# Performance work log

Hardware: AMD Instinct MI355X
Metric: run time of the kernel (lower is better)

The kernel has to match this reference:

```python
import jax, jax.numpy as jnp
import numpy as np

# Dimensions
B, N_PER_MOL = 256, 64            # molecules, atoms per molecule (equal-split case of tf.split)
N = B * N_PER_MOL                 # total atoms
P = 131072                        # total pairs (edges)
D_ATOM, D_PAIR = 256, 64
C = 128                           # num_clusters
H = 50                            # WeaveLayer default hidden sizes (AA=PA=AP=PP=50)
H_A = 2 * H                       # n_hidden_A = n_hidden_AA + n_hidden_PA


def _glorot(key, shape):
    fan_in, fan_out = shape
    lim = jnp.sqrt(6.0 / (fan_in + fan_out)).astype(jnp.float32)
    return jax.random.uniform(key, shape, jnp.float32, -lim, lim)


def setup_inputs() -> dict:
    key = jax.random.key(0)
    ks = jax.random.split(key, 12)
    atom_features = jax.random.normal(ks[0], (N, D_ATOM), jnp.float32)
    pair_features = jax.random.normal(ks[1], (P, D_PAIR), jnp.float32)
    pair_split = jax.random.randint(ks[2], (P,), 0, N, jnp.int32)
    atom_to_pair = jax.random.randint(ks[3], (P, 2), 0, N, jnp.int32)
    num_atoms = jnp.full((B,), N_PER_MOL, dtype=jnp.int32)  # equal-sized molecules
    params = {
        "W_aa": _glorot(ks[4], (D_ATOM, H_A)), "b_aa": jnp.zeros((H_A,), jnp.float32),
        "W_pa": _glorot(ks[5], (D_PAIR, H)),   "b_pa": jnp.zeros((H,), jnp.float32),
        "W_ao": _glorot(ks[6], (H_A + H, C)),  "b_ao": jnp.zeros((C,), jnp.float32),
        "W_ap": _glorot(ks[7], (2 * D_ATOM, H)), "b_ap": jnp.zeros((H,), jnp.float32),
        "W_pp": _glorot(ks[8], (D_PAIR, H)),   "b_pp": jnp.zeros((H,), jnp.float32),
        "W_po": _glorot(ks[9], (2 * H, D_PAIR)), "b_po": jnp.zeros((D_PAIR,), jnp.float32),
    }
    return dict(atom_features=atom_features, pair_features=pair_features,
                pair_split=pair_split, atom_to_pair=atom_to_pair,
                num_atoms=num_atoms, **params)


def reference(atom_features, pair_features, pair_split, atom_to_pair, num_atoms,
              W_aa, b_aa, W_pa, b_pa, W_ao, b_ao, W_ap, b_ap, W_pp, b_pp, W_po, b_po):
    relu = jax.nn.relu
    n_atoms, d_atom = atom_features.shape
    n_mols = num_atoms.shape[0]
    n_per = n_atoms // n_mols  # equal-sized molecules (static)

    # --- WeaveLayer atom path ---
    AA = relu(atom_features @ W_aa + b_aa)                              # [N, 100]
    PA = relu(pair_features @ W_pa + b_pa)                              # [P, 50]
    PA = jax.ops.segment_sum(PA, pair_split, num_segments=n_atoms)     # [N, 50]
    A = relu(jnp.concatenate([AA, PA], axis=-1) @ W_ao + b_ao)          # [N, C] assign logits

    # --- WeaveLayer pair path (computed by the original layer) ---
    ap_ij = atom_features[atom_to_pair].reshape(-1, 2 * d_atom)         # [P, 2D]
    ap_ji = atom_features[atom_to_pair[:, ::-1]].reshape(-1, 2 * d_atom)
    AP = relu(ap_ij @ W_ap + b_ap) + relu(ap_ji @ W_ap + b_ap)          # [P, 50]
    PP = relu(pair_features @ W_pp + b_pp)                              # [P, 50]
    P_out = relu(jnp.concatenate([AP, PP], axis=-1) @ W_po + b_po)      # [P, pair_dim]

    # --- DiffPool: softmax assignment + per-molecule S^T X pooling ---
    assign = jax.nn.softmax(A, axis=-1)                                 # [N, C]
    S = assign.reshape(n_mols, n_per, -1)                               # [B, n, C]
    X = atom_features.reshape(n_mols, n_per, d_atom)                    # [B, n, D]
    pooled = jnp.einsum('bnc,bnd->bcd', S, X)                           # [B, C, D]
    return pooled, P_out
```

## Files before the change

### kernel.cpp

```cpp
#include <hip/hip_runtime.h>
#include <hip/hip_bf16.h>

#define N_ATOMS 16384
#define N_PAIRS 131072

#define OFF_PA    0
#define OFF_PASEG 6815744
#define OFF_AA    7634944
#define OFF_U     9273344
#define OFF_V     10125312
#define OFF_S     10977280
#define OFF_IDX   13074432
#define OFF_OFS   13205504
#define OFF_CNT   13221890

__global__ __launch_bounds__(256) void k0_count(const int* __restrict__ split,
                                                int* __restrict__ cnt)
{
    int p = blockIdx.x * 256 + threadIdx.x;
    atomicAdd(&cnt[split[p]], 1);
}

__global__ __launch_bounds__(1024) void k_scan(int* __restrict__ cnt,
                                               int* __restrict__ ofs)
{
    __shared__ int part[1024];
    const int t = threadIdx.x;
    const int base = t * 16;
    int v[16];
    int s = 0;
    #pragma unroll
    for (int i = 0; i < 16; ++i) { v[i] = cnt[base + i]; s += v[i]; }
    part[t] = s;
    __syncthreads();
    for (int off = 1; off < 1024; off <<= 1) {
        int x = (t >= off) ? part[t - off] : 0;
        __syncthreads();
        part[t] += x;
        __syncthreads();
    }
    int excl = part[t] - s;
    #pragma unroll
    for (int i = 0; i < 16; ++i) {
        int c = v[i];
        ofs[base + i] = excl;
        cnt[base + i] = excl;
        excl += c;
    }
    if (t == 1023) ofs[16384] = excl;
}

__global__ __launch_bounds__(256) void k0_fill(const int* __restrict__ split,
                                               int* __restrict__ cur,
                                               int* __restrict__ idx)
{
    int p = blockIdx.x * 256 + threadIdx.x;
    int pos = atomicAdd(&cur[split[p]], 1);
    idx[pos] = p;
}

__global__ __launch_bounds__(256, 2) void k1_atom(
    const float* __restrict__ X,
    const float* __restrict__ Waa, const float* __restrict__ baa,
    const float* __restrict__ Wap,
    float* __restrict__ AA, float* __restrict__ U, float* __restrict__ V)
{
    __shared__ __align__(16) float xt[256][20];
    const int t = threadIdx.x;
    const int a0 = blockIdx.x * 16;
    #pragma unroll
    for (int r = 0; r < 16; ++r) {
        xt[t][r] = X[(size_t)(a0 + r) * 256 + t];
    }
    __syncthreads();
    const int c = t;
    if (c < 200) {
        const float* wp; int stride; float bias = 0.f;
        if (c < 100)      { wp = Waa + c;                  stride = 100; bias = baa[c]; }
        else if (c < 150) { wp = Wap + (c - 100);          stride = 50; }
        else              { wp = Wap + 256*50 + (c - 150); stride = 50; }
        float acc[16];
        #pragma unroll
        for (int a = 0; a < 16; ++a) acc[a] = bias;
        #pragma unroll 4
        for (int k = 0; k < 256; ++k) {
            float w = wp[(size_t)k * stride];
            const float4* xr = (const float4*)&xt[k][0];
            #pragma unroll
            for (int a4 = 0; a4 < 4; ++a4) {
                float4 x = xr[a4];
                acc[a4*4+0] = fmaf(x.x, w, acc[a4*4+0]);
                acc[a4*4+1] = fmaf(x.y, w, acc[a4*4+1]);
                acc[a4*4+2] = fmaf(x.z, w, acc[a4*4+2]);
                acc[a4*4+3] = fmaf(x.w, w, acc[a4*4+3]);
            }
        }
        if (c < 100) {
            #pragma unroll
            for (int a = 0; a < 16; ++a)
                AA[(size_t)(a0 + a) * 100 + c] = fmaxf(acc[a], 0.f);
        } else if (c < 150) {
            #pragma unroll
            for (int a = 0; a < 16; ++a)
                U[(size_t)(a0 + a) * 52 + (c - 100)] = acc[a];
        } else {
            #pragma unroll
            for (int a = 0; a < 16; ++a)
                V[(size_t)(a0 + a) * 52 + (c - 150)] = acc[a];
        }
    } else if (c == 200) {
        #pragma unroll
        for (int a = 0; a < 16; ++a) {
            U[(size_t)(a0 + a) * 52 + 50] = 0.f;
            U[(size_t)(a0 + a) * 52 + 51] = 0.f;
        }
    } else if (c == 201) {
        #pragma unroll
        for (int a = 0; a < 16; ++a) {
            V[(size_t)(a0 + a) * 52 + 50] = 0.f;
            V[(size_t)(a0 + a) * 52 + 51] = 0.f;
        }
    }
}

__global__ __launch_bounds__(256, 2) void k2a_pa(
    const float* __restrict__ PF,
    const float* __restrict__ Wpa, const float* __restrict__ bpa,
    float* __restrict__ PAo)
{
    __shared__ __align__(16) float Wc[64][52];
    __shared__ __align__(16) float bc[52];
    const int t = threadIdx.x;
    for (int i = t; i < 64 * 52; i += 256) {
        int k = i / 52, c = i % 52;
        Wc[k][c] = (c < 50) ? Wpa[k * 50 + c] : 0.f;
    }
    if (t < 52) bc[t] = (t < 50) ? bpa[t] : 0.f;
    __syncthreads();
    const int p = blockIdx.x * 256 + t;
    float acc[52];
    #pragma unroll
    for (int c = 0; c < 52; ++c) acc[c] = bc[c];
    const float4* pf4 = (const float4*)(PF + (size_t)p * 64);
    #pragma unroll 2
    for (int k4 = 0; k4 < 16; ++k4) {
        float4 xv = pf4[k4];
        float xs[4] = {xv.x, xv.y, xv.z, xv.w};
        #pragma unroll
        for (int kk = 0; kk < 4; ++kk) {
            const float4* wr = (const float4*)&Wc[k4*4 + kk][0];
            float x = xs[kk];
            #pragma unroll
            for (int c4 = 0; c4 < 13; ++c4) {
                float4 w = wr[c4];
                acc[c4*4+0] = fmaf(x, w.x, acc[c4*4+0]);
                acc[c4*4+1] = fmaf(x, w.y, acc[c4*4+1]);
                acc[c4*4+2] = fmaf(x, w.z, acc[c4*4+2]);
                acc[c4*4+3] = fmaf(x, w.w, acc[c4*4+3]);
            }
        }
    }
    float4* op = (float4*)(PAo + (size_t)p * 52);
    #pragma unroll
    for (int q = 0; q < 13; ++q) {
        op[q] = make_float4(fmaxf(acc[4*q+0], 0.f), fmaxf(acc[4*q+1], 0.f),
                            fmaxf(acc[4*q+2], 0.f), fmaxf(acc[4*q+3], 0.f));
    }
}

__global__ __launch_bounds__(256) void k_seg(
    const float* __restrict__ PAo, const int* __restrict__ idx,
    const int* __restrict__ ofs, float* __restrict__ PAseg)
{
    const int t = threadIdx.x;
    const int a = blockIdx.x * 4 + (t >> 6);
    const int lane = t & 63;
    const int beg = ofs[a], end = ofs[a + 1];
    const int cn = end - beg;
    int pre = (lane < cn) ? idx[beg + lane] : 0;
    float s = 0.f;
    for (int j = 0; j < cn; ++j) {
        int p = (j < 64) ? __shfl(pre, j, 64) : idx[beg + j];
        if (lane < 50) s += PAo[(size_t)p * 52 + lane];
    }
    if (lane < 50) PAseg[(size_t)a * 50 + lane] = s;
}

__global__ __launch_bounds__(256, 2) void k2b_pair_out(
    const int* __restrict__ a2p,
    const float* __restrict__ U, const float* __restrict__ V,
    const float* __restrict__ bap_g,
    const float* __restrict__ PF,
    const float* __restrict__ Wpp, const float* __restrict__ bpp_g,
    const float* __restrict__ Wpo, const float* __restrict__ bpo,
    float* __restrict__ Pout)
{
    __shared__ __align__(16) float Wo[100][32];
    __shared__ __align__(16) float Wp[64][52];
    __shared__ __align__(16) float bap[52];
    __shared__ __align__(16) float bpp[52];
    __shared__ float bo[32];
    const int t = threadIdx.x;
    const int h = blockIdx.x & 1;
    const int pb = blockIdx.x >> 1;
    for (int i = t; i < 3200; i += 256)
        Wo[i >> 5][i & 31] = Wpo[(size_t)(i >> 5) * 64 + h * 32 + (i & 31)];
    for (int i = t; i < 64 * 52; i += 256) {
        int k = i / 52, c = i % 52;
        Wp[k][c] = (c < 50) ? Wpp[k * 50 + c] : 0.f;
    }
    if (t < 52) bap[t] = (t < 50) ? bap_g[t] : 0.f;
    if (t < 52) bpp[t] = (t < 50) ? bpp_g[t] : 0.f;
    if (t < 32) bo[t] = bpo[h * 32 + t];
    __syncthreads();
    const int p = pb * 256 + t;

    float pp[52];
    #pragma unroll
    for (int c = 0; c < 52; ++c) pp[c] = bpp[c];
    {
        const float4* pf4 = (const float4*)(PF + (size_t)p * 64);
        #pragma unroll 2
        for (int k4 = 0; k4 < 16; ++k4) {
            float4 xv = pf4[k4];
            float xs[4] = {xv.x, xv.y, xv.z, xv.w};
            #pragma unroll
            for (int kk = 0; kk < 4; ++kk) {
                const float4* wr = (const float4*)&Wp[k4*4 + kk][0];
                float x = xs[kk];
                #pragma unroll
                for (int c4 = 0; c4 < 13; ++c4) {
                    float4 w = wr[c4];
                    pp[c4*4+0] = fmaf(x, w.x, pp[c4*4+0]);
                    pp[c4*4+1] = fmaf(x, w.y, pp[c4*4+1]);
                    pp[c4*4+2] = fmaf(x, w.z, pp[c4*4+2]);
                    pp[c4*4+3] = fmaf(x, w.w, pp[c4*4+3]);
                }
            }
        }
        #pragma unroll
        for (int c = 0; c < 52; ++c) pp[c] = fmaxf(pp[c], 0.f);
    }

    float ap[52];
    {
        const int2 ij = ((const int2*)a2p)[p];
        const float4* Ui = (const float4*)(U + (size_t)ij.x * 52);
        const float4* Vi = (const float4*)(V + (size_t)ij.x * 52);
        const float4* Uj = (const float4*)(U + (size_t)ij.y * 52);
        const float4* Vj = (const float4*)(V + (size_t)ij.y * 52);
        #pragma unroll
        for (int c4 = 0; c4 < 13; ++c4) {
            float4 ui = Ui[c4], vj = Vj[c4], uj = Uj[c4], vi = Vi[c4];
            const float4 bb = *(const float4*)&bap[c4*4];
            ap[c4*4+0] = fmaxf(ui.x + vj.x + bb.x, 0.f) + fmaxf(uj.x + vi.x + bb.x, 0.f);
            ap[c4*4+1] = fmaxf(ui.y + vj.y + bb.y, 0.f) + fmaxf(uj.y + vi.y + bb.y, 0.f);
            ap[c4*4+2] = fmaxf(ui.z + vj.z + bb.z, 0.f) + fmaxf(uj.z + vi.z + bb.z, 0.f);
            ap[c4*4+3] = fmaxf(ui.w + vj.w + bb.w, 0.f) + fmaxf(uj.w + vi.w + bb.w, 0.f);
        }
    }

    float o[32];
    #pragma unroll
    for (int c = 0; c < 32; ++c) o[c] = bo[c];
    #pragma unroll
    for (int k = 0; k < 50; ++k) {
        float a = ap[k];
        const float4* wr = (const float4*)&Wo[k][0];
        #pragma unroll
        for (int c4 = 0; c4 < 8; ++c4) {
            float4 w = wr[c4];
            o[c4*4+0] = fmaf(a, w.x, o[c4*4+0]);
            o[c4*4+1] = fmaf(a, w.y, o[c4*4+1]);
            o[c4*4+2] = fmaf(a, w.z, o[c4*4+2]);
            o[c4*4+3] = fmaf(a, w.w, o[c4*4+3]);
        }
    }
    #pragma unroll
    for (int k = 0; k < 50; ++k) {
        float a = pp[k];
        const float4* wr = (const float4*)&Wo[50 + k][0];
        #pragma unroll
        for (int c4 = 0; c4 < 8; ++c4) {
            float4 w = wr[c4];
            o[c4*4+0] = fmaf(a, w.x, o[c4*4+0]);
            o[c4*4+1] = fmaf(a, w.y, o[c4*4+1]);
            o[c4*4+2] = fmaf(a, w.z, o[c4*4+2]);
            o[c4*4+3] = fmaf(a, w.w, o[c4*4+3]);
        }
    }
    float4* outp = (float4*)(Pout + (size_t)p * 64 + h * 32);
    #pragma unroll
    for (int q = 0; q < 8; ++q) {
        outp[q] = make_float4(fmaxf(o[4*q+0], 0.f), fmaxf(o[4*q+1], 0.f),
                              fmaxf(o[4*q+2], 0.f), fmaxf(o[4*q+3], 0.f));
    }
}

__global__ __launch_bounds__(256, 2) void k3_assign(
    const float* __restrict__ AA, const float* __restrict__ PAseg,
    const float* __restrict__ Wao, const float* __restrict__ bao,
    float* __restrict__ S)
{
    __shared__ __align__(16) float featT[150][16];
    __shared__ __align__(16) float L[16][128];
    const int t = threadIdx.x;
    const int a0 = blockIdx.x * 16;
    for (int idx = t; idx < 2400; idx += 256) {
        int a = idx / 150, k = idx % 150;
        featT[k][a] = (k < 100) ? AA[(size_t)(a0 + a) * 100 + k]
                                : PAseg[(size_t)(a0 + a) * 50 + (k - 100)];
    }
    __syncthreads();
    const int c = t & 127, g = t >> 7;
    float acc[8];
    float b = bao[c];
    #pragma unroll
    for (int a = 0; a < 8; ++a) acc[a] = b;
    #pragma unroll 2
    for (int k = 0; k < 150; ++k) {
        float w = Wao[(size_t)k * 128 + c];
        const float4* fr = (const float4*)&featT[k][g * 8];
        float4 f0 = fr[0], f1 = fr[1];
        acc[0] = fmaf(f0.x, w, acc[0]); acc[1] = fmaf(f0.y, w, acc[1]);
        acc[2] = fmaf(f0.z, w, acc[2]); acc[3] = fmaf(f0.w, w, acc[3]);
        acc[4] = fmaf(f1.x, w, acc[4]); acc[5] = fmaf(f1.y, w, acc[5]);
        acc[6] = fmaf(f1.z, w, acc[6]); acc[7] = fmaf(f1.w, w, acc[7]);
    }
    #pragma unroll
    for (int a = 0; a < 8; ++a) L[g*8 + a][c] = fmaxf(acc[a], 0.f);
    __syncthreads();
    const int r = t & 15, a = t >> 4;
    float v[8];
    #pragma unroll
    for (int q = 0; q < 8; ++q) v[q] = L[a][r + 16*q];
    float m = v[0];
    #pragma unroll
    for (int q = 1; q < 8; ++q) m = fmaxf(m, v[q]);
    #pragma unroll
    for (int w = 1; w < 16; w <<= 1) m = fmaxf(m, __shfl_xor(m, w, 64));
    float e[8];
    float s = 0.f;
    #pragma unroll
    for (int q = 0; q < 8; ++q) { e[q] = __expf(v[q] - m); s += e[q]; }
    #pragma unroll
    for (int w = 1; w < 16; w <<= 1) s += __shfl_xor(s, w, 64);
    float inv = 1.f / s;
    #pragma unroll
    for (int q = 0; q < 8; ++q)
        S[(size_t)(a0 + a) * 128 + r + 16*q] = e[q] * inv;
}

__global__ __launch_bounds__(256, 2) void k4_pool(
    const float* __restrict__ X, const float* __restrict__ S,
    float* __restrict__ pooled)
{
    __shared__ __align__(16) float Sl[64][128];
    __shared__ __align__(16) float Xl[64][64];
    const int t = threadIdx.x;
    const int b = blockIdx.x >> 2;
    const int doff = (blockIdx.x & 3) * 64;
    for (int i = t; i < 8192; i += 256) {
        int n = i >> 7, cd = i & 127;
        Sl[n][cd] = S[(size_t)(b*64 + n) * 128 + cd];
    }
    for (int i = t; i < 4096; i += 256) {
        int n = i >> 6, cd = i & 63;
        Xl[n][cd] = X[(size_t)(b*64 + n) * 256 + doff + cd];
    }
    __syncthreads();
    const int c = t & 127, dq = t >> 7;
    float4 f[8];
    #pragma unroll
    for (int q = 0; q < 8; ++q) f[q] = make_float4(0.f, 0.f, 0.f, 0.f);
    #pragma unroll 2
    for (int n = 0; n < 64; ++n) {
        float s = Sl[n][c];
        const float4* xr = (const float4*)&Xl[n][dq * 32];
        #pragma unroll
        for (int q = 0; q < 8; ++q) {
            float4 x = xr[q];
            f[q].x = fmaf(s, x.x, f[q].x);
            f[q].y = fmaf(s, x.y, f[q].y);
            f[q].z = fmaf(s, x.z, f[q].z);
            f[q].w = fmaf(s, x.w, f[q].w);
        }
    }
    size_t base = (size_t)b * 32768 + (size_t)c * 256 + doff + dq * 32;
    float4* op = (float4*)(pooled + base);
    #pragma unroll
    for (int q = 0; q < 8; ++q) op[q] = f[q];
}

extern "C" void kernel_launch(void* const* d_in, const int* in_sizes, int n_in,
                              void* d_out, int out_size, void* d_ws, size_t ws_size,
                              hipStream_t stream)
{
    const float* atom = (const float*)d_in[0];
    const float* pair = (const float*)d_in[1];
    const int*   split = (const int*)d_in[2];
    const int*   a2p  = (const int*)d_in[3];
    const float* Waa = (const float*)d_in[5];
    const float* baa = (const float*)d_in[6];
    const float* Wpa = (const float*)d_in[7];
    const float* bpa = (const float*)d_in[8];
    const float* Wao = (const float*)d_in[9];
    const float* bao = (const float*)d_in[10];
    const float* Wap = (const float*)d_in[11];
    const float* bap = (const float*)d_in[12];
    const float* Wpp = (const float*)d_in[13];
    const float* bpp = (const float*)d_in[14];
    const float* Wpo = (const float*)d_in[15];
    const float* bpo = (const float*)d_in[16];

    float* ws = (float*)d_ws;
    float* PAo   = ws + OFF_PA;
    float* PAseg = ws + OFF_PASEG;
    float* AA = ws + OFF_AA;
    float* U  = ws + OFF_U;
    float* V  = ws + OFF_V;
    float* Sm = ws + OFF_S;
    int* idx = (int*)(ws + OFF_IDX);
    int* ofs = (int*)(ws + OFF_OFS);
    int* cnt = (int*)(ws + OFF_CNT);

    float* pooled = (float*)d_out;
    float* Pout = pooled + (size_t)256 * 128 * 256;

    hipMemsetAsync(cnt, 0, N_ATOMS * sizeof(int), stream);
    k0_count<<<512, 256, 0, stream>>>(split, cnt);
    k_scan<<<1, 1024, 0, stream>>>(cnt, ofs);
    k0_fill<<<512, 256, 0, stream>>>(split, cnt, idx);
    k1_atom<<<1024, 256, 0, stream>>>(atom, Waa, baa, Wap, AA, U, V);
    k2a_pa<<<512, 256, 0, stream>>>(pair, Wpa, bpa, PAo);
    k_seg<<<4096, 256, 0, stream>>>(PAo, idx, ofs, PAseg);
    k2b_pair_out<<<1024, 256, 0, stream>>>(a2p, U, V, bap, pair, Wpp, bpp, Wpo, bpo, Pout);
    k3_assign<<<1024, 256, 0, stream>>>(AA, PAseg, Wao, bao, Sm);
    k4_pool<<<1024, 256, 0, stream>>>(atom, Sm, pooled);
}
```

Baseline: 427.4 us.

## Drop LDS staging, read weights and activations from global/cache, pre-pad weights once

Removes shared-memory staging from several kernels (atom matmul, pair projections, assign, pool) and reads weights and inputs straight from global memory, relying on cache and uniform loads. Padded copies of the pair weights and biases are built once in the scan kernel instead of in every block. The pair-output kernel now computes both output halves per thread, which halves the grid and avoids recomputing the PP and AP terms twice. The risk is that uncoalesced or strided global reads (e.g. AA and PAseg row reads in assign, per-thread X rows in k1) replace cheap LDS reads, and register pressure rises.

```diff
diff --git a/kernel.cpp b/kernel.cpp
--- a/kernel.cpp
+++ b/kernel.cpp
@@ -13,6 +13,11 @@
 #define OFF_IDX   13074432
 #define OFF_OFS   13205504
 #define OFF_CNT   13221890
+#define OFF_WPAP  13238288
+#define OFF_WPPP  13241616
+#define OFF_BPAP  13244944
+#define OFF_BAPP  13245008
+#define OFF_BPPP  13245072
 
 __global__ __launch_bounds__(256) void k0_count(const int* __restrict__ split,
                                                 int* __restrict__ cnt)
@@ -21,8 +26,13 @@
     atomicAdd(&cnt[split[p]], 1);
 }
 
-__global__ __launch_bounds__(1024) void k_scan(int* __restrict__ cnt,
-                                               int* __restrict__ ofs)
+__global__ __launch_bounds__(1024) void k_scan(
+    int* __restrict__ cnt, int* __restrict__ ofs,
+    const float* __restrict__ Wpa, const float* __restrict__ bpa,
+    const float* __restrict__ Wpp, const float* __restrict__ bpp,
+    const float* __restrict__ bap,
+    float* __restrict__ WpaP, float* __restrict__ WppP,
+    float* __restrict__ BpaP, float* __restrict__ BppP, float* __restrict__ BapP)
 {
     __shared__ int part[1024];
     const int t = threadIdx.x;
@@ -48,6 +58,16 @@
         excl += c;
     }
     if (t == 1023) ofs[16384] = excl;
+    for (int i = t; i < 64 * 52; i += 1024) {
+        int k = i / 52, c = i % 52;
+        WpaP[i] = (c < 50) ? Wpa[k * 50 + c] : 0.f;
+        WppP[i] = (c < 50) ? Wpp[k * 50 + c] : 0.f;
+    }
+    if (t < 52) {
+        BpaP[t] = (t < 50) ? bpa[t] : 0.f;
+        BppP[t] = (t < 50) ? bpp[t] : 0.f;
+        BapP[t] = (t < 50) ? bap[t] : 0.f;
+    }
 }
 
 __global__ __launch_bounds__(256) void k0_fill(const int* __restrict__ split,
@@ -59,100 +79,93 @@
     idx[pos] = p;
 }
 
-__global__ __launch_bounds__(256, 2) void k1_atom(
+__global__ __launch_bounds__(256) void k1_atom(
     const float* __restrict__ X,
     const float* __restrict__ Waa, const float* __restrict__ baa,
     const float* __restrict__ Wap,
     float* __restrict__ AA, float* __restrict__ U, float* __restrict__ V)
 {
-    __shared__ __align__(16) float xt[256][20];
     const int t = threadIdx.x;
     const int a0 = blockIdx.x * 16;
-    #pragma unroll
-    for (int r = 0; r < 16; ++r) {
-        xt[t][r] = X[(size_t)(a0 + r) * 256 + t];
-    }
-    __syncthreads();
     const int c = t;
-    if (c < 200) {
-        const float* wp; int stride; float bias = 0.f;
-        if (c < 100)      { wp = Waa + c;                  stride = 100; bias = baa[c]; }
-        else if (c < 150) { wp = Wap + (c - 100);          stride = 50; }
-        else              { wp = Wap + 256*50 + (c - 150); stride = 50; }
-        float acc[16];
-        #pragma unroll
-        for (int a = 0; a < 16; ++a) acc[a] = bias;
-        #pragma unroll 4
-        for (int k = 0; k < 256; ++k) {
-            float w = wp[(size_t)k * stride];
-            const float4* xr = (const float4*)&xt[k][0];
-            #pragma unroll
-            for (int a4 = 0; a4 < 4; ++a4) {
-                float4 x = xr[a4];
-                acc[a4*4+0] = fmaf(x.x, w, acc[a4*4+0]);
-                acc[a4*4+1] = fmaf(x.y, w, acc[a4*4+1]);
-                acc[a4*4+2] = fmaf(x.z, w, acc[a4*4+2]);
-                acc[a4*4+3] = fmaf(x.w, w, acc[a4*4+3]);
-            }
-        }
-        if (c < 100) {
-            #pragma unroll
-            for (int a = 0; a < 16; ++a)
-                AA[(size_t)(a0 + a) * 100 + c] = fmaxf(acc[a], 0.f);
-        } else if (c < 150) {
-            #pragma unroll
-            for (int a = 0; a < 16; ++a)
-                U[(size_t)(a0 + a) * 52 + (c - 100)] = acc[a];
-        } else {
-            #pragma unroll
-            for (int a = 0; a < 16; ++a)
-                V[(size_t)(a0 + a) * 52 + (c - 150)] = acc[a];
-        }
-    } else if (c == 200) {
+    if (c >= 202) return;
+    if (c == 200) {
         #pragma unroll
         for (int a = 0; a < 16; ++a) {
             U[(size_t)(a0 + a) * 52 + 50] = 0.f;
             U[(size_t)(a0 + a) * 52 + 51] = 0.f;
         }
-    } else if (c == 201) {
+        return;
+    }
+    if (c == 201) {
         #pragma unroll
         for (int a = 0; a < 16; ++a) {
             V[(size_t)(a0 + a) * 52 + 50] = 0.f;
             V[(size_t)(a0 + a) * 52 + 51] = 0.f;
         }
-    }
-}
-
-__global__ __launch_bounds__(256, 2) void k2a_pa(
+        return;
+    }
+    const float* wp; int stride; float bias = 0.f;
+    if (c < 100)      { wp = Waa + c;                  stride = 100; bias = baa[c]; }
+    else if (c < 150) { wp = Wap + (c - 100);          stride = 50; }
+    else              { wp = Wap + 256*50 + (c - 150); stride = 50; }
+    float acc[16];
+    #pragma unroll
+    for (int a = 0; a < 16; ++a) acc[a] = bias;
+    for (int k4 = 0; k4 < 64; ++k4) {
+        float4 xq[16];
+        #pragma unroll
+        for (int r = 0; r < 16; ++r)
+            xq[r] = *(const float4*)(X + (size_t)(a0 + r) * 256 + k4 * 4);
+        #pragma unroll
+        for (int kk = 0; kk < 4; ++kk) {
+            float w = wp[(size_t)(k4 * 4 + kk) * stride];
+            #pragma unroll
+            for (int r = 0; r < 16; ++r) {
+                float xv = (kk == 0) ? xq[r].x : (kk == 1) ? xq[r].y
+                         : (kk == 2) ? xq[r].z : xq[r].w;
+                acc[r] = fmaf(xv, w, acc[r]);
+            }
+        }
+    }
+    if (c < 100) {
+        #pragma unroll
+        for (int a = 0; a < 16; ++a)
+            AA[(size_t)(a0 + a) * 100 + c] = fmaxf(acc[a], 0.f);
+    } else if (c < 150) {
+        #pragma unroll
+        for (int a = 0; a < 16; ++a)
+            U[(size_t)(a0 + a) * 52 + (c - 100)] = acc[a];
+    } else {
+        #pragma unroll
+        for (int a = 0; a < 16; ++a)
+            V[(size_t)(a0 + a) * 52 + (c - 150)] = acc[a];
+    }
+}
+
+__global__ __launch_bounds__(256) void k2a_pa(
     const float* __restrict__ PF,
-    const float* __restrict__ Wpa, const float* __restrict__ bpa,
+    const float* __restrict__ WpaP, const float* __restrict__ BpaP,
     float* __restrict__ PAo)
 {
-    __shared__ __align__(16) float Wc[64][52];
-    __shared__ __align__(16) float bc[52];
-    const int t = threadIdx.x;
-    for (int i = t; i < 64 * 52; i += 256) {
-        int k = i / 52, c = i % 52;
-        Wc[k][c] = (c < 50) ? Wpa[k * 50 + c] : 0.f;
-    }
-    if (t < 52) bc[t] = (t < 50) ? bpa[t] : 0.f;
-    __syncthreads();
+    const int t = threadIdx.x;
     const int p = blockIdx.x * 256 + t;
     float acc[52];
     #pragma unroll
-    for (int c = 0; c < 52; ++c) acc[c] = bc[c];
+    for (int c4 = 0; c4 < 13; ++c4) {
+        float4 b = *(const float4*)(BpaP + c4 * 4);
+        acc[c4*4+0] = b.x; acc[c4*4+1] = b.y; acc[c4*4+2] = b.z; acc[c4*4+3] = b.w;
+    }
     const float4* pf4 = (const float4*)(PF + (size_t)p * 64);
-    #pragma unroll 2
     for (int k4 = 0; k4 < 16; ++k4) {
         float4 xv = pf4[k4];
-        float xs[4] = {xv.x, xv.y, xv.z, xv.w};
         #pragma unroll
         for (int kk = 0; kk < 4; ++kk) {
-            const float4* wr = (const float4*)&Wc[k4*4 + kk][0];
-            float x = xs[kk];
+            float x = (kk == 0) ? xv.x : (kk == 1) ? xv.y : (kk == 2) ? xv.z : xv.w;
+            const float* wr = WpaP + (k4 * 4 + kk) * 52;
             #pragma unroll
             for (int c4 = 0; c4 < 13; ++c4) {
-                float4 w = wr[c4];
+                float4 w = *(const float4*)(wr + c4 * 4);
                 acc[c4*4+0] = fmaf(x, w.x, acc[c4*4+0]);
                 acc[c4*4+1] = fmaf(x, w.y, acc[c4*4+1]);
                 acc[c4*4+2] = fmaf(x, w.z, acc[c4*4+2]);
@@ -189,48 +202,32 @@
 __global__ __launch_bounds__(256, 2) void k2b_pair_out(
     const int* __restrict__ a2p,
     const float* __restrict__ U, const float* __restrict__ V,
-    const float* __restrict__ bap_g,
+    const float* __restrict__ BapP,
     const float* __restrict__ PF,
-    const float* __restrict__ Wpp, const float* __restrict__ bpp_g,
+    const float* __restrict__ WppP, const float* __restrict__ BppP,
     const float* __restrict__ Wpo, const float* __restrict__ bpo,
     float* __restrict__ Pout)
 {
-    __shared__ __align__(16) float Wo[100][32];
-    __shared__ __align__(16) float Wp[64][52];
-    __shared__ __align__(16) float bap[52];
-    __shared__ __align__(16) float bpp[52];
-    __shared__ float bo[32];
-    const int t = threadIdx.x;
-    const int h = blockIdx.x & 1;
-    const int pb = blockIdx.x >> 1;
-    for (int i = t; i < 3200; i += 256)
-        Wo[i >> 5][i & 31] = Wpo[(size_t)(i >> 5) * 64 + h * 32 + (i & 31)];
-    for (int i = t; i < 64 * 52; i += 256) {
-        int k = i / 52, c = i % 52;
-        Wp[k][c] = (c < 50) ? Wpp[k * 50 + c] : 0.f;
-    }
-    if (t < 52) bap[t] = (t < 50) ? bap_g[t] : 0.f;
-    if (t < 52) bpp[t] = (t < 50) ? bpp_g[t] : 0.f;
-    if (t < 32) bo[t] = bpo[h * 32 + t];
-    __syncthreads();
-    const int p = pb * 256 + t;
+    const int t = threadIdx.x;
+    const int p = blockIdx.x * 256 + t;
 
     float pp[52];
     #pragma unroll
-    for (int c = 0; c < 52; ++c) pp[c] = bpp[c];
+    for (int c4 = 0; c4 < 13; ++c4) {
+        float4 b = *(const float4*)(BppP + c4 * 4);
+        pp[c4*4+0] = b.x; pp[c4*4+1] = b.y; pp[c4*4+2] = b.z; pp[c4*4+3] = b.w;
+    }
     {
         const float4* pf4 = (const float4*)(PF + (size_t)p * 64);
-        #pragma unroll 2
         for (int k4 = 0; k4 < 16; ++k4) {
             float4 xv = pf4[k4];
-            float xs[4] = {xv.x, xv.y, xv.z, xv.w};
             #pragma unroll
             for (int kk = 0; kk < 4; ++kk) {
-                const float4* wr = (const float4*)&Wp[k4*4 + kk][0];
-                float x = xs[kk];
+                float x = (kk == 0) ? xv.x : (kk == 1) ? xv.y : (kk == 2) ? xv.z : xv.w;
+                const float* wr = WppP + (k4 * 4 + kk) * 52;
                 #pragma unroll
                 for (int c4 = 0; c4 < 13; ++c4) {
-                    float4 w = wr[c4];
+                    float4 w = *(const float4*)(wr + c4 * 4);
                     pp[c4*4+0] = fmaf(x, w.x, pp[c4*4+0]);
                     pp[c4*4+1] = fmaf(x, w.y, pp[c4*4+1]);
                     pp[c4*4+2] = fmaf(x, w.z, pp[c4*4+2]);
@@ -252,7 +249,7 @@
         #pragma unroll
         for (int c4 = 0; c4 < 13; ++c4) {
             float4 ui = Ui[c4], vj = Vj[c4], uj = Uj[c4], vi = Vi[c4];
-            const float4 bb = *(const float4*)&bap[c4*4];
+            const float4 bb = *(const float4*)(BapP + c4 * 4);
             ap[c4*4+0] = fmaxf(ui.x + vj.x + bb.x, 0.f) + fmaxf(uj.x + vi.x + bb.x, 0.f);
             ap[c4*4+1] = fmaxf(ui.y + vj.y + bb.y, 0.f) + fmaxf(uj.y + vi.y + bb.y, 0.f);
             ap[c4*4+2] = fmaxf(ui.z + vj.z + bb.z, 0.f) + fmaxf(uj.z + vi.z + bb.z, 0.f);
@@ -260,40 +257,46 @@
         }
     }
 
-    float o[32];
-    #pragma unroll
-    for (int c = 0; c < 32; ++c) o[c] = bo[c];
-    #pragma unroll
-    for (int k = 0; k < 50; ++k) {
-        float a = ap[k];
-        const float4* wr = (const float4*)&Wo[k][0];
-        #pragma unroll
-        for (int c4 = 0; c4 < 8; ++c4) {
-            float4 w = wr[c4];
-            o[c4*4+0] = fmaf(a, w.x, o[c4*4+0]);
-            o[c4*4+1] = fmaf(a, w.y, o[c4*4+1]);
-            o[c4*4+2] = fmaf(a, w.z, o[c4*4+2]);
-            o[c4*4+3] = fmaf(a, w.w, o[c4*4+3]);
-        }
-    }
-    #pragma unroll
-    for (int k = 0; k < 50; ++k) {
-        float a = pp[k];
-        const float4* wr = (const float4*)&Wo[50 + k][0];
-        #pragma unroll
-        for (int c4 = 0; c4 < 8; ++c4) {
-            float4 w = wr[c4];
-            o[c4*4+0] = fmaf(a, w.x, o[c4*4+0]);
-            o[c4*4+1] = fmaf(a, w.y, o[c4*4+1]);
-            o[c4*4+2] = fmaf(a, w.z, o[c4*4+2]);
-            o[c4*4+3] = fmaf(a, w.w, o[c4*4+3]);
-        }
-    }
-    float4* outp = (float4*)(Pout + (size_t)p * 64 + h * 32);
-    #pragma unroll
-    for (int q = 0; q < 8; ++q) {
-        outp[q] = make_float4(fmaxf(o[4*q+0], 0.f), fmaxf(o[4*q+1], 0.f),
-                              fmaxf(o[4*q+2], 0.f), fmaxf(o[4*q+3], 0.f));
+    float4* outp = (float4*)(Pout + (size_t)p * 64);
+    #pragma unroll 1
+    for (int h = 0; h < 2; ++h) {
+        float o[32];
+        #pragma unroll
+        for (int q = 0; q < 8; ++q) {
+            float4 b = *(const float4*)(bpo + h * 32 + q * 4);
+            o[q*4+0] = b.x; o[q*4+1] = b.y; o[q*4+2] = b.z; o[q*4+3] = b.w;
+        }
+        #pragma unroll
+        for (int k = 0; k < 50; ++k) {
+            float a = ap[k];
+            const float* wr = Wpo + k * 64 + h * 32;
+            #pragma unroll
+            for (int c4 = 0; c4 < 8; ++c4) {
+                float4 w = *(const float4*)(wr + c4 * 4);
+                o[c4*4+0] = fmaf(a, w.x, o[c4*4+0]);
+                o[c4*4+1] = fmaf(a, w.y, o[c4*4+1]);
+                o[c4*4+2] = fmaf(a, w.z, o[c4*4+2]);
+                o[c4*4+3] = fmaf(a, w.w, o[c4*4+3]);
+            }
+        }
+        #pragma unroll
+        for (int k = 0; k < 50; ++k) {
+            float a = pp[k];
+            const float* wr = Wpo + (50 + k) * 64 + h * 32;
+            #pragma unroll
+            for (int c4 = 0; c4 < 8; ++c4) {
+                float4 w = *(const float4*)(wr + c4 * 4);
+                o[c4*4+0] = fmaf(a, w.x, o[c4*4+0]);
+                o[c4*4+1] = fmaf(a, w.y, o[c4*4+1]);
+                o[c4*4+2] = fmaf(a, w.z, o[c4*4+2]);
+                o[c4*4+3] = fmaf(a, w.w, o[c4*4+3]);
+            }
+        }
+        #pragma unroll
+        for (int q = 0; q < 8; ++q) {
+            outp[h*8 + q] = make_float4(fmaxf(o[4*q+0], 0.f), fmaxf(o[4*q+1], 0.f),
+                                        fmaxf(o[4*q+2], 0.f), fmaxf(o[4*q+3], 0.f));
+        }
     }
 }
 
@@ -302,30 +305,29 @@
     const float* __restrict__ Wao, const float* __restrict__ bao,
     float* __restrict__ S)
 {
-    __shared__ __align__(16) float featT[150][16];
     __shared__ __align__(16) float L[16][128];
     const int t = threadIdx.x;
     const int a0 = blockIdx.x * 16;
-    for (int idx = t; idx < 2400; idx += 256) {
-        int a = idx / 150, k = idx % 150;
-        featT[k][a] = (k < 100) ? AA[(size_t)(a0 + a) * 100 + k]
-                                : PAseg[(size_t)(a0 + a) * 50 + (k - 100)];
-    }
-    __syncthreads();
     const int c = t & 127, g = t >> 7;
     float acc[8];
     float b = bao[c];
     #pragma unroll
     for (int a = 0; a < 8; ++a) acc[a] = b;
-    #pragma unroll 2
-    for (int k = 0; k < 150; ++k) {
+    for (int k = 0; k < 100; ++k) {
         float w = Wao[(size_t)k * 128 + c];
-        const float4* fr = (const float4*)&featT[k][g * 8];
-        float4 f0 = fr[0], f1 = fr[1];
-        acc[0] = fmaf(f0.x, w, acc[0]); acc[1] = fmaf(f0.y, w, acc[1]);
-        acc[2] = fmaf(f0.z, w, acc[2]); acc[3] = fmaf(f0.w, w, acc[3]);
-        acc[4] = fmaf(f1.x, w, acc[4]); acc[5] = fmaf(f1.y, w, acc[5]);
-        acc[6] = fmaf(f1.z, w, acc[6]); acc[7] = fmaf(f1.w, w, acc[7]);
+        #pragma unroll
+        for (int j = 0; j < 8; ++j) {
+            float f = AA[(size_t)(a0 + g*8 + j) * 100 + k];
+            acc[j] = fmaf(f, w, acc[j]);
+        }
+    }
+    for (int k = 0; k < 50; ++k) {
+        float w = Wao[(size_t)(100 + k) * 128 + c];
+        #pragma unroll
+        for (int j = 0; j < 8; ++j) {
+            float f = PAseg[(size_t)(a0 + g*8 + j) * 50 + k];
+            acc[j] = fmaf(f, w, acc[j]);
+        }
     }
     #pragma unroll
     for (int a = 0; a < 8; ++a) L[g*8 + a][c] = fmaxf(acc[a], 0.f);
@@ -356,7 +358,6 @@
     float* __restrict__ pooled)
 {
     __shared__ __align__(16) float Sl[64][128];
-    __shared__ __align__(16) float Xl[64][64];
     const int t = threadIdx.x;
     const int b = blockIdx.x >> 2;
     const int doff = (blockIdx.x & 3) * 64;
@@ -364,22 +365,17 @@
         int n = i >> 7, cd = i & 127;
         Sl[n][cd] = S[(size_t)(b*64 + n) * 128 + cd];
     }
-    for (int i = t; i < 4096; i += 256) {
-        int n = i >> 6, cd = i & 63;
-        Xl[n][cd] = X[(size_t)(b*64 + n) * 256 + doff + cd];
-    }
     __syncthreads();
     const int c = t & 127, dq = t >> 7;
     float4 f[8];
     #pragma unroll
     for (int q = 0; q < 8; ++q) f[q] = make_float4(0.f, 0.f, 0.f, 0.f);
-    #pragma unroll 2
     for (int n = 0; n < 64; ++n) {
         float s = Sl[n][c];
-        const float4* xr = (const float4*)&Xl[n][dq * 32];
+        const float* xr = X + (size_t)(b*64 + n) * 256 + doff + dq * 32;
         #pragma unroll
         for (int q = 0; q < 8; ++q) {
-            float4 x = xr[q];
+            float4 x = *(const float4*)(xr + q * 4);
             f[q].x = fmaf(s, x.x, f[q].x);
             f[q].y = fmaf(s, x.y, f[q].y);
             f[q].z = fmaf(s, x.z, f[q].z);
@@ -423,18 +419,25 @@
     int* idx = (int*)(ws + OFF_IDX);
     int* ofs = (int*)(ws + OFF_OFS);
     int* cnt = (int*)(ws + OFF_CNT);
+    float* WpaP = ws + OFF_WPAP;
+    float* WppP = ws + OFF_WPPP;
+    float* BpaP = ws + OFF_BPAP;
+    float* BapP = ws + OFF_BAPP;
+    float* BppP = ws + OFF_BPPP;
 
     float* pooled = (float*)d_out;
     float* Pout = pooled + (size_t)256 * 128 * 256;
 
     hipMemsetAsync(cnt, 0, N_ATOMS * sizeof(int), stream);
     k0_count<<<512, 256, 0, stream>>>(split, cnt);
-    k_scan<<<1, 1024, 0, stream>>>(cnt, ofs);
+    k_scan<<<1, 1024, 0, stream>>>(cnt, ofs, Wpa, bpa, Wpp, bpp, bap,
+                                   WpaP, WppP, BpaP, BppP, BapP);
     k0_fill<<<512, 256, 0, stream>>>(split, cnt, idx);
     k1_atom<<<1024, 256, 0, stream>>>(atom, Waa, baa, Wap, AA, U, V);
-    k2a_pa<<<512, 256, 0, stream>>>(pair, Wpa, bpa, PAo);
+    k2a_pa<<<512, 256, 0, stream>>>(pair, WpaP, BpaP, PAo);
     k_seg<<<4096, 256, 0, stream>>>(PAo, idx, ofs, PAseg);
-    k2b_pair_out<<<1024, 256, 0, stream>>>(a2p, U, V, bap, pair, Wpp, bpp, Wpo, bpo, Pout);
+    k2b_pair_out<<<512, 256, 0, stream>>>(a2p, U, V, BapP, pair, WppP, BppP,
+                                          Wpo, bpo, Pout);
     k3_assign<<<1024, 256, 0, stream>>>(AA, PAseg, Wao, bao, Sm);
     k4_pool<<<1024, 256, 0, stream>>>(atom, Sm, pooled);
 }
```

Measured after the change: 555.2 us. 1.3x slower.
